# Performance work log

Measured on AMD Instinct MI355X. Metric: run time of the kernel, lower is better.

The kernel has to match this reference:

```python
import jax, jax.numpy as jnp
import numpy as np

B, N, C = 16, 1024, 256
NH, DH = 8, 32          # dense attention heads
NHD, P = 8, 4           # deformable heads / sampling points
Hs = Ws = 32            # value spatial grid (N == Hs*Ws)
HID = 1024              # mlp hidden = 4*C


def setup_inputs() -> dict:
    key = jax.random.key(0)
    ks = jax.random.split(key, 16)
    rn = lambda i, shape, s=1.0: jax.random.normal(ks[i], shape, jnp.float32) * s
    return {
        "x": rn(0, (B, N, C)),
        "ref": jax.random.uniform(ks[1], (B, N, 2), jnp.float32),
        "value": rn(2, (B, N, C)),
        "ln1_w": jnp.ones((C,), jnp.float32), "ln1_b": jnp.zeros((C,), jnp.float32),
        "ln2_w": jnp.ones((C,), jnp.float32), "ln2_b": jnp.zeros((C,), jnp.float32),
        "ln3_w": jnp.ones((C,), jnp.float32), "ln3_b": jnp.zeros((C,), jnp.float32),
        "qkv_w": rn(3, (3 * C, C), 0.05),
        "proj_w": rn(4, (C, C), 0.05), "proj_b": jnp.zeros((C,), jnp.float32),
        "off_w": rn(5, (NHD * P * 2, C), 0.01), "off_b": rn(6, (NHD * P * 2,), 0.5),
        "aw_w": rn(7, (NHD * P, C), 0.01), "aw_b": jnp.zeros((NHD * P,), jnp.float32),
        "vproj_w": rn(8, (C, C), 0.05), "vproj_b": jnp.zeros((C,), jnp.float32),
        "oproj_w": rn(9, (C, C), 0.05), "oproj_b": jnp.zeros((C,), jnp.float32),
        "fc1_w": rn(10, (HID, C), 0.05), "fc1_b": jnp.zeros((HID,), jnp.float32),
        "fc2_w": rn(11, (C, HID), 0.05), "fc2_b": jnp.zeros((C,), jnp.float32),
    }


def _ln(x, w, b):
    m = x.mean(-1, keepdims=True)
    v = ((x - m) ** 2).mean(-1, keepdims=True)
    return (x - m) * jax.lax.rsqrt(v + 1e-5) * w + b


def _attn(x, qkv_w, proj_w, proj_b):
    qkv = (x @ qkv_w.T).reshape(B, N, 3, NH, DH)
    q, k, v = qkv[:, :, 0], qkv[:, :, 1], qkv[:, :, 2]
    a = jnp.einsum('bqhd,bkhd->bhqk', q, k) * (DH ** -0.5)
    a = jax.nn.softmax(a, axis=-1)
    o = jnp.einsum('bhqk,bkhd->bqhd', a, v).reshape(B, N, C)
    return o @ proj_w.T + proj_b


def _deform(q, ref, value, off_w, off_b, aw_w, aw_b, vproj_w, vproj_b, oproj_w, oproj_b):
    # single-level MS deformable attention (Deformable-DETR style)
    v = (value @ vproj_w.T + vproj_b).reshape(B, Hs * Ws, NHD, DH)
    off = (q @ off_w.T + off_b).reshape(B, N, NHD, P, 2)
    aw = jax.nn.softmax((q @ aw_w.T + aw_b).reshape(B, N, NHD, P), axis=-1)
    norm = jnp.array([Ws, Hs], jnp.float32)
    loc = ref[:, :, None, None, :] + off / norm  # [B,N,NHD,P,2] normalized coords
    gx = loc[..., 0] * Ws - 0.5
    gy = loc[..., 1] * Hs - 0.5
    x0 = jnp.floor(gx); y0 = jnp.floor(gy)
    lx = gx - x0; ly = gy - y0
    x0i = x0.astype(jnp.int32); y0i = y0.astype(jnp.int32)
    b_idx = jnp.arange(B)[:, None, None, None]
    h_idx = jnp.arange(NHD)[None, None, :, None]

    def gather(xi, yi):
        valid = ((xi >= 0) & (xi < Ws) & (yi >= 0) & (yi < Hs)).astype(jnp.float32)
        idx = jnp.clip(yi, 0, Hs - 1) * Ws + jnp.clip(xi, 0, Ws - 1)
        return v[b_idx, idx, h_idx] * valid[..., None]  # [B,N,NHD,P,DH]

    s = (gather(x0i, y0i) * ((1 - lx) * (1 - ly))[..., None]
         + gather(x0i + 1, y0i) * (lx * (1 - ly))[..., None]
         + gather(x0i, y0i + 1) * ((1 - lx) * ly)[..., None]
         + gather(x0i + 1, y0i + 1) * (lx * ly)[..., None])
    out = (s * aw[..., None]).sum(axis=3).reshape(B, N, C)
    return out @ oproj_w.T + oproj_b


def reference(x, ref, value, ln1_w, ln1_b, ln2_w, ln2_b, ln3_w, ln3_b,
              qkv_w, proj_w, proj_b, off_w, off_b, aw_w, aw_b,
              vproj_w, vproj_b, oproj_w, oproj_b, fc1_w, fc1_b, fc2_w, fc2_b):
    x = x + _attn(_ln(x, ln1_w, ln1_b), qkv_w, proj_w, proj_b)
    x = x + _deform(_ln(x, ln2_w, ln2_b), ref, value,
                    off_w, off_b, aw_w, aw_b, vproj_w, vproj_b, oproj_w, oproj_b)
    h = jax.nn.gelu(_ln(x, ln3_w, ln3_b) @ fc1_w.T + fc1_b, approximate=False) @ fc2_w.T + fc2_b
    return x + h
```

## Files before the change

kernel.cpp:

```cpp
#include <hip/hip_runtime.h>
#include <hip/hip_bf16.h>

#define Bq   16
#define Nq   1024
#define Cq   256
#define NHq  8
#define DHq  32
#define HIDq 1024
#define BNq  (Bq * Nq)

typedef float f32x4 __attribute__((ext_vector_type(4)));
typedef short bf16x8 __attribute__((ext_vector_type(8)));
typedef unsigned short ushort_t;

__device__ __forceinline__ unsigned int f2bf(float f) {
    unsigned int u = __builtin_bit_cast(unsigned int, f);
    u = (u + 0x7fffu + ((u >> 16) & 1u)) >> 16;
    return u & 0xffffu;
}
__device__ __forceinline__ unsigned int packbf2(float a, float b) {
    unsigned int ua = __builtin_bit_cast(unsigned int, a) + 0x8000u;
    unsigned int ub = __builtin_bit_cast(unsigned int, b) + 0x8000u;
    return __builtin_amdgcn_perm(ub, ua, 0x07060302);
}
__device__ __forceinline__ unsigned int cvtpk_bf16(float lo, float hi) {
    unsigned int r;
    asm("v_cvt_pk_bf16_f32 %0, %1, %2" : "=v"(r) : "v"(lo), "v"(hi));
    return r;
}
__device__ __forceinline__ float gelu_t(float x) {
    float y = x * (0.7978845608028654f + 0.035677408136300125f * x * x);
    float e = __builtin_amdgcn_exp2f(y * 2.8853900817779268f);
    return x - x / (1.f + e);
}

typedef __attribute__((address_space(1))) const unsigned int* gas_u32;
typedef __attribute__((address_space(3))) unsigned int* las_u32;
__device__ __forceinline__ void gload16(const void* g, void* l) {
    __builtin_amdgcn_global_load_lds((gas_u32)g, (las_u32)l, 16, 0, 0);
}

struct CastSeg { const float* src; ushort_t* dst; int nblk; int n; };
struct CastArgs { CastSeg s[9]; };

__global__ __launch_bounds__(256) void castm(CastArgs a) {
    int bid = blockIdx.x;
    int seg = 0, acc = 0;
    for (seg = 0; seg < 9; seg++) {
        if (bid < acc + a.s[seg].nblk) break;
        acc += a.s[seg].nblk;
    }
    const CastSeg sg = a.s[seg];
    int i = (bid - acc) * 1024 + threadIdx.x * 4;
    if (i < sg.n) {
        float4 v = *(const float4*)(sg.src + i);
        uint2 u;
        u.x = packbf2(v.x, v.y);
        u.y = packbf2(v.z, v.w);
        *(uint2*)(sg.dst + i) = u;
    }
}

__global__ __launch_bounds__(256) void ln_kernel(const float* __restrict__ X,
                                                 const float* __restrict__ w,
                                                 const float* __restrict__ b,
                                                 ushort_t* __restrict__ Y) {
    int wave = threadIdx.x >> 6, lane = threadIdx.x & 63;
    int t = blockIdx.x * 4 + wave;
    float4 v = *(const float4*)(X + (size_t)t * Cq + lane * 4);
    float s = v.x + v.y + v.z + v.w;
#pragma unroll
    for (int d = 1; d < 64; d <<= 1) s += __shfl_xor(s, d);
    float mean = s * (1.f / 256.f);
    float4 dv = {v.x - mean, v.y - mean, v.z - mean, v.w - mean};
    float q = dv.x * dv.x + dv.y * dv.y + dv.z * dv.z + dv.w * dv.w;
#pragma unroll
    for (int d = 1; d < 64; d <<= 1) q += __shfl_xor(q, d);
    float rs = rsqrtf(q * (1.f / 256.f) + 1e-5f);
    float4 wv = *(const float4*)(w + lane * 4);
    float4 bv = *(const float4*)(b + lane * 4);
    uint2 u;
    u.x = packbf2(dv.x * rs * wv.x + bv.x, dv.y * rs * wv.y + bv.y);
    u.y = packbf2(dv.z * rs * wv.z + bv.z, dv.w * rs * wv.w + bv.w);
    *(uint2*)(Y + (size_t)t * Cq + lane * 4) = u;
}

template <int OMODE, bool GELU_, bool RESID, int KT>
__global__ __launch_bounds__(256) void mgemm(const ushort_t* __restrict__ A,
                                             const ushort_t* __restrict__ W,
                                             const float* __restrict__ bias,
                                             const float* __restrict__ R,
                                             void* __restrict__ OutP,
                                             int M, int Nn) {
    __shared__ __align__(16) ushort_t Al[2][8192];
    __shared__ __align__(16) ushort_t Bl[2][4096];
    int m0 = blockIdx.x * 128, n0 = blockIdx.y * 64;
    int tid = threadIdx.x;
    int w = tid >> 6, lane = tid & 63;
    int l15 = lane & 15, quad = lane >> 4;

    f32x4 acc[2][4];
#pragma unroll
    for (int i = 0; i < 2; i++)
#pragma unroll
        for (int j = 0; j < 4; j++) acc[i][j] = (f32x4){0.f, 0.f, 0.f, 0.f};

    const ushort_t* gA0 = A + (size_t)(m0 + lane) * KT + w * 8;
    const ushort_t* gA1 = gA0 + (size_t)64 * KT;
    const ushort_t* gB0 = W + (size_t)(n0 + lane) * KT + w * 8;

    auto STAGE = [&](int buf, int t) {
        const int k0 = t * 64;
        gload16(gA0 + k0,      &Al[buf][w * 1024]);
        gload16(gA1 + k0,      &Al[buf][w * 1024 + 512]);
        gload16(gA0 + k0 + 32, &Al[buf][(w + 4) * 1024]);
        gload16(gA1 + k0 + 32, &Al[buf][(w + 4) * 1024 + 512]);
        gload16(gB0 + k0,      &Bl[buf][w * 512]);
        gload16(gB0 + k0 + 32, &Bl[buf][(w + 4) * 512]);
    };

    constexpr int NT = KT / 64;
    STAGE(0, 0);
    STAGE(1, 1);
    asm volatile("s_waitcnt vmcnt(6)" ::: "memory");
    __builtin_amdgcn_s_barrier();

#pragma unroll
    for (int t = 0; t < NT; t++) {
        const int cur = t & 1;
        bf16x8 aF[2][2], bF[2][4];
#pragma unroll
        for (int ks = 0; ks < 2; ks++) {
#pragma unroll
            for (int i = 0; i < 2; i++)
                aF[ks][i] = *(const bf16x8*)&Al[cur][(ks * 4 + quad) * 1024 + (w * 32 + i * 16 + l15) * 8];
#pragma unroll
            for (int j = 0; j < 4; j++)
                bF[ks][j] = *(const bf16x8*)&Bl[cur][(ks * 4 + quad) * 512 + (j * 16 + l15) * 8];
        }
        asm volatile("s_waitcnt lgkmcnt(0)" ::: "memory");
        __builtin_amdgcn_sched_barrier(0);
        __builtin_amdgcn_s_barrier();
        if (t + 2 < NT) STAGE(cur, t + 2);

        __builtin_amdgcn_s_setprio(1);
#pragma unroll
        for (int ks = 0; ks < 2; ks++)
#pragma unroll
            for (int i = 0; i < 2; i++)
#pragma unroll
                for (int j = 0; j < 4; j++)
                    acc[i][j] = __builtin_amdgcn_mfma_f32_16x16x32_bf16(bF[ks][j], aF[ks][i], acc[i][j], 0, 0, 0);
        __builtin_amdgcn_s_setprio(0);

        if (t + 2 < NT) {
            asm volatile("s_waitcnt vmcnt(6)" ::: "memory");
        } else if (t + 1 < NT) {
            asm volatile("s_waitcnt vmcnt(0)" ::: "memory");
        }
        if (t + 1 < NT) __builtin_amdgcn_s_barrier();
    }

#pragma unroll
    for (int i = 0; i < 2; i++) {
        int mg = m0 + w * 32 + i * 16 + l15;
#pragma unroll
        for (int j = 0; j < 4; j++) {
            int ng = n0 + j * 16 + quad * 4;
            f32x4 rv = acc[i][j];
            if constexpr (OMODE == 1) {
                int which = ng >> 8;
                int h = (ng >> 5) & 7;
                int d = ng & 31;
                int bb = mg >> 10, nn = mg & 1023;
                ushort_t* qb = (ushort_t*)OutP;
                if (which == 2) {
                    size_t dst = 2 * (size_t)BNq * Cq +
                                 ((size_t)(bb * 8 + h) * 32 + d) * 1024 + nn;
#pragma unroll
                    for (int r = 0; r < 4; r++)
                        qb[dst + (size_t)r * 1024] = (ushort_t)f2bf(rv[r]);
                } else {
                    if (which == 0) {
                        const float sc = 0.17677669529663687f * 1.4426950408889634f;
                        rv[0] *= sc; rv[1] *= sc; rv[2] *= sc; rv[3] *= sc;
                    }
                    size_t dst = (size_t)which * ((size_t)BNq * Cq) +
                                 ((size_t)(bb * 8 + h) * 1024 + nn) * 32 + d;
                    uint2 pk;
                    pk.x = packbf2(rv[0], rv[1]);
                    pk.y = packbf2(rv[2], rv[3]);
                    *(uint2*)(qb + dst) = pk;
                }
            } else if constexpr (OMODE == 3) {
                if (ng >= 96) continue;
                if (ng < 64) {
                    float4 bv = *(const float4*)(bias + ng);
                    rv[0] += bv.x; rv[1] += bv.y; rv[2] += bv.z; rv[3] += bv.w;
                    *(float4*)((float*)OutP + (size_t)mg * 64 + ng) =
                        make_float4(rv[0], rv[1], rv[2], rv[3]);
                } else {
                    float4 bv = *(const float4*)(R + (ng - 64));
                    rv[0] += bv.x; rv[1] += bv.y; rv[2] += bv.z; rv[3] += bv.w;
                    *(float4*)((float*)OutP + (size_t)BNq * 64 + (size_t)mg * 32 + (ng - 64)) =
                        make_float4(rv[0], rv[1], rv[2], rv[3]);
                }
            } else {
                if (bias) {
                    float4 bv = *(const float4*)(bias + ng);
                    rv[0] += bv.x; rv[1] += bv.y; rv[2] += bv.z; rv[3] += bv.w;
                }
                if (GELU_) {
#pragma unroll
                    for (int r = 0; r < 4; r++) rv[r] = gelu_t(rv[r]);
                }
                if constexpr (OMODE == 2) {
                    uint2 pk;
                    pk.x = packbf2(rv[0], rv[1]);
                    pk.y = packbf2(rv[2], rv[3]);
                    *(uint2*)((ushort_t*)OutP + (size_t)mg * Nn + ng) = pk;
                } else {
                    if (RESID) {
                        float4 rr = *(const float4*)(R + (size_t)mg * Nn + ng);
                        rv[0] += rr.x; rv[1] += rr.y; rv[2] += rr.z; rv[3] += rr.w;
                    }
                    *(float4*)((float*)OutP + (size_t)mg * Nn + ng) =
                        make_float4(rv[0], rv[1], rv[2], rv[3]);
                }
            }
        }
    }
}

__global__ __launch_bounds__(256, 4) void attn_mfma(const ushort_t* __restrict__ Qb,
                                                    const ushort_t* __restrict__ Kb,
                                                    const ushort_t* __restrict__ Vtg,
                                                    ushort_t* __restrict__ o) {
    int bh = blockIdx.x;
    int b = bh >> 3, h = bh & 7;
    int q0 = blockIdx.y * 128;
    int tid = threadIdx.x;
    int wave = tid >> 6, lane = tid & 63;
    int l15 = lane & 15, quad = lane >> 4;

    __shared__ __align__(16) ushort_t Ks[2][64][40];
    __shared__ __align__(16) ushort_t Vs[2][32][88];
    __shared__ __align__(16) ushort_t Ps[4][32][72];

    const size_t hb = (size_t)bh * 32768;

    bf16x8 qfrag[2];
#pragma unroll
    for (int g = 0; g < 2; g++)
        qfrag[g] = *(const bf16x8*)(Qb + hb + (size_t)(q0 + wave * 32 + g * 16 + l15) * 32 + quad * 8);

    f32x4 oa[2][2];
#pragma unroll
    for (int g = 0; g < 2; g++)
#pragma unroll
        for (int t = 0; t < 2; t++) oa[g][t] = (f32x4){0.f, 0.f, 0.f, 0.f};
    f32x4 ls[2];
    ls[0] = (f32x4){0.f, 0.f, 0.f, 0.f};
    ls[1] = (f32x4){0.f, 0.f, 0.f, 0.f};

    bf16x8 ones;
#pragma unroll
    for (int i = 0; i < 8; i++) ones[i] = (short)0x3F80;

    int krow = tid >> 2, kch = tid & 3;
    int vrow = tid >> 3, vch = tid & 7;
    const ushort_t* kgp = Kb + hb + (size_t)krow * 32 + kch * 8;
    const ushort_t* vgp = Vtg + hb + (size_t)vrow * 1024 + vch * 8;

    bf16x8 kreg = *(const bf16x8*)kgp;
    bf16x8 vreg = *(const bf16x8*)vgp;

#pragma unroll 2
    for (int kt = 0; kt < 16; kt++) {
        const int cur = kt & 1;
        *(bf16x8*)&Ks[cur][krow][kch * 8] = kreg;
        *(bf16x8*)&Vs[cur][vrow][vch * 8] = vreg;
        __syncthreads();
        if (kt < 15) {
            kreg = *(const bf16x8*)(kgp + (kt + 1) * 2048);
            vreg = *(const bf16x8*)(vgp + (kt + 1) * 64);
        }

        bf16x8 kf[4];
#pragma unroll
        for (int kg = 0; kg < 4; kg++)
            kf[kg] = *(const bf16x8*)&Ks[cur][kg * 16 + l15][quad * 8];

        const f32x4 z = {0.f, 0.f, 0.f, 0.f};
#pragma unroll
        for (int g = 0; g < 2; g++) {
#pragma unroll
            for (int kg = 0; kg < 4; kg++) {
                f32x4 st = __builtin_amdgcn_mfma_f32_16x16x32_bf16(kf[kg], qfrag[g], z, 0, 0, 0);
                float e0 = __builtin_amdgcn_exp2f(st[0]);
                float e1 = __builtin_amdgcn_exp2f(st[1]);
                float e2 = __builtin_amdgcn_exp2f(st[2]);
                float e3 = __builtin_amdgcn_exp2f(st[3]);
                uint2 pk;
                pk.x = cvtpk_bf16(e0, e1);
                pk.y = cvtpk_bf16(e2, e3);
                *(uint2*)&Ps[wave][g * 16 + l15][kg * 16 + quad * 4] = pk;
            }
        }

        __builtin_amdgcn_s_setprio(1);
#pragma unroll
        for (int c = 0; c < 2; c++) {
            bf16x8 vb0 = *(const bf16x8*)&Vs[cur][l15][c * 32 + quad * 8];
            bf16x8 vb1 = *(const bf16x8*)&Vs[cur][16 + l15][c * 32 + quad * 8];
#pragma unroll
            for (int g = 0; g < 2; g++) {
                bf16x8 pa = *(const bf16x8*)&Ps[wave][g * 16 + l15][c * 32 + quad * 8];
                oa[g][0] = __builtin_amdgcn_mfma_f32_16x16x32_bf16(pa, vb0, oa[g][0], 0, 0, 0);
                oa[g][1] = __builtin_amdgcn_mfma_f32_16x16x32_bf16(pa, vb1, oa[g][1], 0, 0, 0);
                ls[g]    = __builtin_amdgcn_mfma_f32_16x16x32_bf16(pa, ones, ls[g], 0, 0, 0);
            }
        }
        __builtin_amdgcn_s_setprio(0);
    }

#pragma unroll
    for (int g = 0; g < 2; g++) {
#pragma unroll
        for (int r = 0; r < 4; r++) {
            float inv = 1.f / ls[g][r];
            int q = q0 + wave * 32 + g * 16 + quad * 4 + r;
            ushort_t* orow = o + ((size_t)(b * 1024 + q)) * 256 + h * 32;
            orow[l15] = (ushort_t)f2bf(oa[g][0][r] * inv);
            orow[l15 + 16] = (ushort_t)f2bf(oa[g][1][r] * inv);
        }
    }
}

__global__ __launch_bounds__(256) void deform_kernel(const float* __restrict__ ref,
                                                     const float* __restrict__ off,
                                                     const float* __restrict__ awl,
                                                     const float* __restrict__ v,
                                                     ushort_t* __restrict__ out) {
    int t = blockIdx.x;
    int b = t >> 10;
    int tid = threadIdx.x;
    int h = tid >> 5, d = tid & 31;

    float rx = ref[(size_t)t * 2 + 0];
    float ry = ref[(size_t)t * 2 + 1];
    const float* offr = off + (size_t)t * 64 + h * 8;
    const float* awr = awl + (size_t)t * 32 + h * 4;

    float L0 = awr[0], L1 = awr[1], L2 = awr[2], L3 = awr[3];
    float mm = fmaxf(fmaxf(L0, L1), fmaxf(L2, L3));
    float e0 = __expf(L0 - mm), e1 = __expf(L1 - mm), e2 = __expf(L2 - mm), e3 = __expf(L3 - mm);
    float inv = 1.f / (e0 + e1 + e2 + e3);
    float aw[4] = {e0 * inv, e1 * inv, e2 * inv, e3 * inv};

    const float* vb = v + (size_t)b * Nq * Cq + h * 32 + d;

    float s = 0.f;
#pragma unroll
    for (int p = 0; p < 4; p++) {
        float gx = rx * 32.f + offr[p * 2 + 0] - 0.5f;
        float gy = ry * 32.f + offr[p * 2 + 1] - 0.5f;
        float x0f = floorf(gx), y0f = floorf(gy);
        float lx = gx - x0f, ly = gy - y0f;
        int x0 = (int)x0f, y0 = (int)y0f;
        auto g = [&](int xi, int yi) -> float {
            if (xi < 0 || xi > 31 || yi < 0 || yi > 31) return 0.f;
            return vb[(size_t)(yi * 32 + xi) * Cq];
        };
        float sp = g(x0, y0) * (1.f - lx) * (1.f - ly)
                 + g(x0 + 1, y0) * lx * (1.f - ly)
                 + g(x0, y0 + 1) * (1.f - lx) * ly
                 + g(x0 + 1, y0 + 1) * lx * ly;
        s += aw[p] * sp;
    }
    out[(size_t)t * Cq + h * 32 + d] = (ushort_t)f2bf(s);
}

extern "C" void kernel_launch(void* const* d_in, const int* in_sizes, int n_in,
                              void* d_out, int out_size, void* d_ws, size_t ws_size,
                              hipStream_t stream) {
    const size_t S = (size_t)BNq * Cq;
    float* ws = (float*)d_ws;
    float* X = ws;
    ushort_t* Ybf = (ushort_t*)(ws + S);
    ushort_t* Wbf = (ushort_t*)(ws + S + S / 2);

    ushort_t* Wqkv   = Wbf;
    ushort_t* Wproj  = Wbf + 196608;
    ushort_t* Woff   = Wbf + 262144;
    ushort_t* Waw    = Wbf + 278528;
    ushort_t* Wvproj = Wbf + 286720;
    ushort_t* Woproj = Wbf + 352256;
    ushort_t* Wfc1   = Wbf + 417792;
    ushort_t* Wfc2   = Wbf + 679936;

    ushort_t* QKVbf = (ushort_t*)(ws + 2 * S);
    ushort_t* O1bf  = (ushort_t*)(ws + 2 * S + 3 * S / 2);
    float* Vb   = ws + 2 * S + S / 2;
    float* OffB = ws + 2 * S + 3 * S / 2;
    float* AwB  = OffB + (size_t)BNq * 64;
    ushort_t* Sbbf = (ushort_t*)(AwB + (size_t)BNq * 32);
    ushort_t* Hbbf = (ushort_t*)(ws + 2 * S);
    ushort_t* Valbf = (ushort_t*)(ws + 9 * S / 2);

    auto fp = [&](int i) { return (const float*)d_in[i]; };
    const float* x_in = fp(0);

    CastArgs ca;
    ca.s[0] = {fp(9),  Wqkv,   192, 196608};
    ca.s[1] = {fp(10), Wproj,  64,  65536};
    ca.s[2] = {fp(12), Woff,   16,  16384};
    ca.s[3] = {fp(14), Waw,    8,   8192};
    ca.s[4] = {fp(16), Wvproj, 64,  65536};
    ca.s[5] = {fp(18), Woproj, 64,  65536};
    ca.s[6] = {fp(20), Wfc1,   256, 262144};
    ca.s[7] = {fp(22), Wfc2,   256, 262144};
    ca.s[8] = {fp(2),  Valbf,  4096, (int)S};
    castm<<<5016, 256, 0, stream>>>(ca);

    ln_kernel<<<BNq / 4, 256, 0, stream>>>(x_in, fp(3), fp(4), Ybf);
    mgemm<1, false, false, 256><<<dim3(128, 12), 256, 0, stream>>>(
        Ybf, Wqkv, nullptr, nullptr, QKVbf, BNq, 768);
    attn_mfma<<<dim3(128, 8), 256, 0, stream>>>(
        QKVbf, QKVbf + S, QKVbf + 2 * S, O1bf);
    mgemm<0, false, true, 256><<<dim3(128, 4), 256, 0, stream>>>(
        O1bf, Wproj, fp(11), x_in, X, BNq, 256);

    ln_kernel<<<BNq / 4, 256, 0, stream>>>(X, fp(5), fp(6), Ybf);
    mgemm<0, false, false, 256><<<dim3(128, 4), 256, 0, stream>>>(
        Valbf, Wvproj, fp(17), nullptr, Vb, BNq, 256);
    mgemm<3, false, false, 256><<<dim3(128, 2), 256, 0, stream>>>(
        Ybf, Woff, fp(13), fp(15), OffB, BNq, 96);
    deform_kernel<<<BNq, 256, 0, stream>>>(fp(1), OffB, AwB, Vb, Sbbf);
    mgemm<0, false, true, 256><<<dim3(128, 4), 256, 0, stream>>>(
        Sbbf, Woproj, fp(19), X, X, BNq, 256);

    ln_kernel<<<BNq / 4, 256, 0, stream>>>(X, fp(7), fp(8), Ybf);
    mgemm<2, true, false, 256><<<dim3(128, 16), 256, 0, stream>>>(
        Ybf, Wfc1, fp(21), nullptr, Hbbf, BNq, 1024);
    mgemm<0, false, true, 1024><<<dim3(128, 4), 256, 0, stream>>>(
        Hbbf, Wfc2, fp(23), X, d_out, BNq, 256);
}
```

Baseline: 332.2 us.

## Replace double-buffered GEMM k-loop with large single-stage 256-wide K chunks

The GEMM mainloop drops the two-stage LDS double buffer with explicit vmcnt waits. It now loads an entire 256-wide K chunk of A and W into LDS, synchronises, then runs eight MFMA substeps from LDS. This cuts barriers and wait bookkeeping per K, but global loads no longer overlap compute within a block. LDS use grows to 96 KB, which may reduce occupancy.

```diff
diff --git a/kernel.cpp b/kernel.cpp
--- a/kernel.cpp
+++ b/kernel.cpp
@@ -92,8 +92,8 @@
                                              const float* __restrict__ R,
                                              void* __restrict__ OutP,
                                              int M, int Nn) {
-    __shared__ __align__(16) ushort_t Al[2][8192];
-    __shared__ __align__(16) ushort_t Bl[2][4096];
+    __shared__ __align__(16) ushort_t Al[32768];
+    __shared__ __align__(16) ushort_t Bl[16384];
     int m0 = blockIdx.x * 128, n0 = blockIdx.y * 64;
     int tid = threadIdx.x;
     int w = tid >> 6, lane = tid & 63;
@@ -105,60 +105,43 @@
 #pragma unroll
         for (int j = 0; j < 4; j++) acc[i][j] = (f32x4){0.f, 0.f, 0.f, 0.f};
 
-    const ushort_t* gA0 = A + (size_t)(m0 + lane) * KT + w * 8;
+    const ushort_t* gA0 = A + (size_t)(m0 + lane) * KT;
     const ushort_t* gA1 = gA0 + (size_t)64 * KT;
-    const ushort_t* gB0 = W + (size_t)(n0 + lane) * KT + w * 8;
-
-    auto STAGE = [&](int buf, int t) {
-        const int k0 = t * 64;
-        gload16(gA0 + k0,      &Al[buf][w * 1024]);
-        gload16(gA1 + k0,      &Al[buf][w * 1024 + 512]);
-        gload16(gA0 + k0 + 32, &Al[buf][(w + 4) * 1024]);
-        gload16(gA1 + k0 + 32, &Al[buf][(w + 4) * 1024 + 512]);
-        gload16(gB0 + k0,      &Bl[buf][w * 512]);
-        gload16(gB0 + k0 + 32, &Bl[buf][(w + 4) * 512]);
-    };
-
-    constexpr int NT = KT / 64;
-    STAGE(0, 0);
-    STAGE(1, 1);
-    asm volatile("s_waitcnt vmcnt(6)" ::: "memory");
-    __builtin_amdgcn_s_barrier();
-
-#pragma unroll
-    for (int t = 0; t < NT; t++) {
-        const int cur = t & 1;
-        bf16x8 aF[2][2], bF[2][4];
-#pragma unroll
-        for (int ks = 0; ks < 2; ks++) {
+    const ushort_t* gB0 = W + (size_t)(n0 + lane) * KT;
+
+    constexpr int NC = KT / 256;
+#pragma unroll
+    for (int c = 0; c < NC; c++) {
+        if (c > 0) __syncthreads();
+        const int kb = c * 256;
+#pragma unroll
+        for (int j = 0; j < 8; j++) {
+            const int k = kb + w * 8 + j * 32;
+            const int kc = w + 4 * j;
+            gload16(gA0 + k, &Al[kc * 1024]);
+            gload16(gA1 + k, &Al[kc * 1024 + 512]);
+            gload16(gB0 + k, &Bl[kc * 512]);
+        }
+        __syncthreads();
+
+        __builtin_amdgcn_s_setprio(1);
+#pragma unroll
+        for (int s = 0; s < 8; s++) {
+            const int kc = 4 * s + quad;
+            bf16x8 aF[2], bF[4];
 #pragma unroll
             for (int i = 0; i < 2; i++)
-                aF[ks][i] = *(const bf16x8*)&Al[cur][(ks * 4 + quad) * 1024 + (w * 32 + i * 16 + l15) * 8];
+                aF[i] = *(const bf16x8*)&Al[kc * 1024 + (w * 32 + i * 16 + l15) * 8];
 #pragma unroll
             for (int j = 0; j < 4; j++)
-                bF[ks][j] = *(const bf16x8*)&Bl[cur][(ks * 4 + quad) * 512 + (j * 16 + l15) * 8];
-        }
-        asm volatile("s_waitcnt lgkmcnt(0)" ::: "memory");
-        __builtin_amdgcn_sched_barrier(0);
-        __builtin_amdgcn_s_barrier();
-        if (t + 2 < NT) STAGE(cur, t + 2);
-
-        __builtin_amdgcn_s_setprio(1);
-#pragma unroll
-        for (int ks = 0; ks < 2; ks++)
+                bF[j] = *(const bf16x8*)&Bl[kc * 512 + (j * 16 + l15) * 8];
 #pragma unroll
             for (int i = 0; i < 2; i++)
 #pragma unroll
                 for (int j = 0; j < 4; j++)
-                    acc[i][j] = __builtin_amdgcn_mfma_f32_16x16x32_bf16(bF[ks][j], aF[ks][i], acc[i][j], 0, 0, 0);
+                    acc[i][j] = __builtin_amdgcn_mfma_f32_16x16x32_bf16(bF[j], aF[i], acc[i][j], 0, 0, 0);
+        }
         __builtin_amdgcn_s_setprio(0);
-
-        if (t + 2 < NT) {
-            asm volatile("s_waitcnt vmcnt(6)" ::: "memory");
-        } else if (t + 1 < NT) {
-            asm volatile("s_waitcnt vmcnt(0)" ::: "memory");
-        }
-        if (t + 1 < NT) __builtin_amdgcn_s_barrier();
     }
 
 #pragma unroll
```

After: 377.3 us. 1.14x slower.

## Triple-buffer GEMM LDS pipeline and remap block IDs per XCD

Applied to the files above, without the earlier changes.

The shared mgemm kernel moves from double to triple-buffered LDS staging, prefetching three K-tiles ahead and adjusting vmcnt waits to match. It also switches to a 1D grid with an XCD-aware remap, so the 16 consecutive M-tiles handled by each XCD share weight tiles in that XCD's L2. The aim is to hide more global load latency and improve cache locality. The cost is 50% more LDS per block, which may lower occupancy. With KT=256 there are only four K-tiles, so the deeper prefetch gives little room to overlap.

```diff
diff --git a/kernel.cpp b/kernel.cpp
--- a/kernel.cpp
+++ b/kernel.cpp
@@ -12,6 +12,10 @@
 typedef float f32x4 __attribute__((ext_vector_type(4)));
 typedef short bf16x8 __attribute__((ext_vector_type(8)));
 typedef unsigned short ushort_t;
+
+#define VMW12() asm volatile("s_waitcnt vmcnt(12)" ::: "memory")
+#define VMW6()  asm volatile("s_waitcnt vmcnt(6)" ::: "memory")
+#define VMW0()  asm volatile("s_waitcnt vmcnt(0)" ::: "memory")
 
 __device__ __forceinline__ unsigned int f2bf(float f) {
     unsigned int u = __builtin_bit_cast(unsigned int, f);
@@ -92,9 +96,13 @@
                                              const float* __restrict__ R,
                                              void* __restrict__ OutP,
                                              int M, int Nn) {
-    __shared__ __align__(16) ushort_t Al[2][8192];
-    __shared__ __align__(16) ushort_t Bl[2][4096];
-    int m0 = blockIdx.x * 128, n0 = blockIdx.y * 64;
+    __shared__ __align__(16) ushort_t Al[3][8192];
+    __shared__ __align__(16) ushort_t Bl[3][4096];
+    int L = blockIdx.x;
+    int xcd = L & 7, idx = L >> 3;
+    int bx = xcd * 16 + (idx & 15);
+    int by = idx >> 4;
+    int m0 = bx * 128, n0 = by * 64;
     int tid = threadIdx.x;
     int w = tid >> 6, lane = tid & 63;
     int l15 = lane & 15, quad = lane >> 4;
@@ -122,12 +130,14 @@
     constexpr int NT = KT / 64;
     STAGE(0, 0);
     STAGE(1, 1);
-    asm volatile("s_waitcnt vmcnt(6)" ::: "memory");
+    STAGE(2, 2);
+    VMW12();
     __builtin_amdgcn_s_barrier();
+    __builtin_amdgcn_sched_barrier(0);
 
 #pragma unroll
     for (int t = 0; t < NT; t++) {
-        const int cur = t & 1;
+        const int cur = t % 3;
         bf16x8 aF[2][2], bF[2][4];
 #pragma unroll
         for (int ks = 0; ks < 2; ks++) {
@@ -141,7 +151,8 @@
         asm volatile("s_waitcnt lgkmcnt(0)" ::: "memory");
         __builtin_amdgcn_sched_barrier(0);
         __builtin_amdgcn_s_barrier();
-        if (t + 2 < NT) STAGE(cur, t + 2);
+        __builtin_amdgcn_sched_barrier(0);
+        if (t + 3 < NT) STAGE(cur, t + 3);
 
         __builtin_amdgcn_s_setprio(1);
 #pragma unroll
@@ -153,12 +164,14 @@
                     acc[i][j] = __builtin_amdgcn_mfma_f32_16x16x32_bf16(bF[ks][j], aF[ks][i], acc[i][j], 0, 0, 0);
         __builtin_amdgcn_s_setprio(0);
 
-        if (t + 2 < NT) {
-            asm volatile("s_waitcnt vmcnt(6)" ::: "memory");
-        } else if (t + 1 < NT) {
-            asm volatile("s_waitcnt vmcnt(0)" ::: "memory");
-        }
-        if (t + 1 < NT) __builtin_amdgcn_s_barrier();
+        if (t + 1 < NT) {
+            const int rem = ((t + 3 < NT ? t + 3 : NT - 1)) - (t + 1);
+            if (rem >= 2)      { VMW12(); }
+            else if (rem == 1) { VMW6(); }
+            else               { VMW0(); }
+            __builtin_amdgcn_s_barrier();
+            __builtin_amdgcn_sched_barrier(0);
+        }
     }
 
 #pragma unroll
@@ -424,25 +437,25 @@
     castm<<<5016, 256, 0, stream>>>(ca);
 
     ln_kernel<<<BNq / 4, 256, 0, stream>>>(x_in, fp(3), fp(4), Ybf);
-    mgemm<1, false, false, 256><<<dim3(128, 12), 256, 0, stream>>>(
+    mgemm<1, false, false, 256><<<128 * 12, 256, 0, stream>>>(
         Ybf, Wqkv, nullptr, nullptr, QKVbf, BNq, 768);
     attn_mfma<<<dim3(128, 8), 256, 0, stream>>>(
         QKVbf, QKVbf + S, QKVbf + 2 * S, O1bf);
-    mgemm<0, false, true, 256><<<dim3(128, 4), 256, 0, stream>>>(
+    mgemm<0, false, true, 256><<<128 * 4, 256, 0, stream>>>(
         O1bf, Wproj, fp(11), x_in, X, BNq, 256);
 
     ln_kernel<<<BNq / 4, 256, 0, stream>>>(X, fp(5), fp(6), Ybf);
-    mgemm<0, false, false, 256><<<dim3(128, 4), 256, 0, stream>>>(
+    mgemm<0, false, false, 256><<<128 * 4, 256, 0, stream>>>(
         Valbf, Wvproj, fp(17), nullptr, Vb, BNq, 256);
-    mgemm<3, false, false, 256><<<dim3(128, 2), 256, 0, stream>>>(
+    mgemm<3, false, false, 256><<<128 * 2, 256, 0, stream>>>(
         Ybf, Woff, fp(13), fp(15), OffB, BNq, 96);
     deform_kernel<<<BNq, 256, 0, stream>>>(fp(1), OffB, AwB, Vb, Sbbf);
-    mgemm<0, false, true, 256><<<dim3(128, 4), 256, 0, stream>>>(
+    mgemm<0, false, true, 256><<<128 * 4, 256, 0, stream>>>(
         Sbbf, Woproj, fp(19), X, X, BNq, 256);
 
     ln_kernel<<<BNq / 4, 256, 0, stream>>>(X, fp(7), fp(8), Ybf);
-    mgemm<2, true, false, 256><<<dim3(128, 16), 256, 0, stream>>>(
+    mgemm<2, true, false, 256><<<128 * 16, 256, 0, stream>>>(
         Ybf, Wfc1, fp(21), nullptr, Hbbf, BNq, 1024);
-    mgemm<0, false, true, 1024><<<dim3(128, 4), 256, 0, stream>>>(
+    mgemm<0, false, true, 1024><<<128 * 4, 256, 0, stream>>>(
         Hbbf, Wfc2, fp(23), X, d_out, BNq, 256);
 }
```

New measurement: 339.3 us. 2.1% more time.

## Process multiple M-tiles per GEMM block with continuous cross-tile prefetch pipeline

Applied to the files above, without the earlier changes.

The mgemm kernel gains an NTILES template parameter so each block processes several consecutive 128-row M tiles. The double-buffered load pipeline runs across tile boundaries, so loads for the next tile are issued while the current one finishes and its epilogue runs. The QKV GEMM uses 2 tiles per block and fc1 uses 4, which shrinks their grids. This is meant to amortise pipeline prologue/drain and launch overhead, at the cost of fewer blocks and therefore less parallelism across the GPU.

```diff
diff --git a/kernel.cpp b/kernel.cpp
--- a/kernel.cpp
+++ b/kernel.cpp
@@ -12,6 +12,9 @@
 typedef float f32x4 __attribute__((ext_vector_type(4)));
 typedef short bf16x8 __attribute__((ext_vector_type(8)));
 typedef unsigned short ushort_t;
+
+#define VMW6()  asm volatile("s_waitcnt vmcnt(6)" ::: "memory")
+#define VMW0()  asm volatile("s_waitcnt vmcnt(0)" ::: "memory")
 
 __device__ __forceinline__ unsigned int f2bf(float f) {
     unsigned int u = __builtin_bit_cast(unsigned int, f);
@@ -85,7 +88,7 @@
     *(uint2*)(Y + (size_t)t * Cq + lane * 4) = u;
 }
 
-template <int OMODE, bool GELU_, bool RESID, int KT>
+template <int OMODE, bool GELU_, bool RESID, int KT, int NTILES>
 __global__ __launch_bounds__(256) void mgemm(const ushort_t* __restrict__ A,
                                              const ushort_t* __restrict__ W,
                                              const float* __restrict__ bias,
@@ -94,7 +97,9 @@
                                              int M, int Nn) {
     __shared__ __align__(16) ushort_t Al[2][8192];
     __shared__ __align__(16) ushort_t Bl[2][4096];
-    int m0 = blockIdx.x * 128, n0 = blockIdx.y * 64;
+    constexpr int NT = KT / 64;
+    constexpr int TOT = NT * NTILES;
+    int m_base = blockIdx.x * (128 * NTILES), n0 = blockIdx.y * 64;
     int tid = threadIdx.x;
     int w = tid >> 6, lane = tid & 63;
     int l15 = lane & 15, quad = lane >> 4;
@@ -105,29 +110,101 @@
 #pragma unroll
         for (int j = 0; j < 4; j++) acc[i][j] = (f32x4){0.f, 0.f, 0.f, 0.f};
 
-    const ushort_t* gA0 = A + (size_t)(m0 + lane) * KT + w * 8;
+    const ushort_t* gA0 = A + (size_t)(m_base + lane) * KT + w * 8;
     const ushort_t* gA1 = gA0 + (size_t)64 * KT;
     const ushort_t* gB0 = W + (size_t)(n0 + lane) * KT + w * 8;
 
-    auto STAGE = [&](int buf, int t) {
-        const int k0 = t * 64;
-        gload16(gA0 + k0,      &Al[buf][w * 1024]);
-        gload16(gA1 + k0,      &Al[buf][w * 1024 + 512]);
-        gload16(gA0 + k0 + 32, &Al[buf][(w + 4) * 1024]);
-        gload16(gA1 + k0 + 32, &Al[buf][(w + 4) * 1024 + 512]);
-        gload16(gB0 + k0,      &Bl[buf][w * 512]);
-        gload16(gB0 + k0 + 32, &Bl[buf][(w + 4) * 512]);
+    auto STAGE = [&](int buf, int u) {
+        const size_t aoff = (size_t)(u / NT) * 128 * KT + (u % NT) * 64;
+        const int k0 = (u % NT) * 64;
+        gload16(gA0 + aoff,      &Al[buf][w * 1024]);
+        gload16(gA1 + aoff,      &Al[buf][w * 1024 + 512]);
+        gload16(gA0 + aoff + 32, &Al[buf][(w + 4) * 1024]);
+        gload16(gA1 + aoff + 32, &Al[buf][(w + 4) * 1024 + 512]);
+        gload16(gB0 + k0,        &Bl[buf][w * 512]);
+        gload16(gB0 + k0 + 32,   &Bl[buf][(w + 4) * 512]);
     };
 
-    constexpr int NT = KT / 64;
+    auto EPI = [&](int tile) {
+#pragma unroll
+        for (int i = 0; i < 2; i++) {
+            int mg = m_base + tile * 128 + w * 32 + i * 16 + l15;
+#pragma unroll
+            for (int j = 0; j < 4; j++) {
+                int ng = n0 + j * 16 + quad * 4;
+                f32x4 rv = acc[i][j];
+                if constexpr (OMODE == 1) {
+                    int which = ng >> 8;
+                    int h = (ng >> 5) & 7;
+                    int d = ng & 31;
+                    int bb = mg >> 10, nn = mg & 1023;
+                    ushort_t* qb = (ushort_t*)OutP;
+                    if (which == 2) {
+                        size_t dst = 2 * (size_t)BNq * Cq +
+                                     ((size_t)(bb * 8 + h) * 32 + d) * 1024 + nn;
+#pragma unroll
+                        for (int r = 0; r < 4; r++)
+                            qb[dst + (size_t)r * 1024] = (ushort_t)f2bf(rv[r]);
+                    } else {
+                        if (which == 0) {
+                            const float sc = 0.17677669529663687f * 1.4426950408889634f;
+                            rv[0] *= sc; rv[1] *= sc; rv[2] *= sc; rv[3] *= sc;
+                        }
+                        size_t dst = (size_t)which * ((size_t)BNq * Cq) +
+                                     ((size_t)(bb * 8 + h) * 1024 + nn) * 32 + d;
+                        uint2 pk;
+                        pk.x = packbf2(rv[0], rv[1]);
+                        pk.y = packbf2(rv[2], rv[3]);
+                        *(uint2*)(qb + dst) = pk;
+                    }
+                } else if constexpr (OMODE == 3) {
+                    if (ng >= 96) continue;
+                    if (ng < 64) {
+                        float4 bv = *(const float4*)(bias + ng);
+                        rv[0] += bv.x; rv[1] += bv.y; rv[2] += bv.z; rv[3] += bv.w;
+                        *(float4*)((float*)OutP + (size_t)mg * 64 + ng) =
+                            make_float4(rv[0], rv[1], rv[2], rv[3]);
+                    } else {
+                        float4 bv = *(const float4*)(R + (ng - 64));
+                        rv[0] += bv.x; rv[1] += bv.y; rv[2] += bv.z; rv[3] += bv.w;
+                        *(float4*)((float*)OutP + (size_t)BNq * 64 + (size_t)mg * 32 + (ng - 64)) =
+                            make_float4(rv[0], rv[1], rv[2], rv[3]);
+                    }
+                } else {
+                    if (bias) {
+                        float4 bv = *(const float4*)(bias + ng);
+                        rv[0] += bv.x; rv[1] += bv.y; rv[2] += bv.z; rv[3] += bv.w;
+                    }
+                    if (GELU_) {
+#pragma unroll
+                        for (int r = 0; r < 4; r++) rv[r] = gelu_t(rv[r]);
+                    }
+                    if constexpr (OMODE == 2) {
+                        uint2 pk;
+                        pk.x = packbf2(rv[0], rv[1]);
+                        pk.y = packbf2(rv[2], rv[3]);
+                        *(uint2*)((ushort_t*)OutP + (size_t)mg * Nn + ng) = pk;
+                    } else {
+                        if (RESID) {
+                            float4 rr = *(const float4*)(R + (size_t)mg * Nn + ng);
+                            rv[0] += rr.x; rv[1] += rr.y; rv[2] += rr.z; rv[3] += rr.w;
+                        }
+                        *(float4*)((float*)OutP + (size_t)mg * Nn + ng) =
+                            make_float4(rv[0], rv[1], rv[2], rv[3]);
+                    }
+                }
+            }
+        }
+    };
+
     STAGE(0, 0);
     STAGE(1, 1);
-    asm volatile("s_waitcnt vmcnt(6)" ::: "memory");
+    VMW6();
     __builtin_amdgcn_s_barrier();
 
 #pragma unroll
-    for (int t = 0; t < NT; t++) {
-        const int cur = t & 1;
+    for (int s = 0; s < TOT; s++) {
+        const int cur = s & 1;
         bf16x8 aF[2][2], bF[2][4];
 #pragma unroll
         for (int ks = 0; ks < 2; ks++) {
@@ -141,7 +218,7 @@
         asm volatile("s_waitcnt lgkmcnt(0)" ::: "memory");
         __builtin_amdgcn_sched_barrier(0);
         __builtin_amdgcn_s_barrier();
-        if (t + 2 < NT) STAGE(cur, t + 2);
+        if (s + 2 < TOT) STAGE(cur, s + 2);
 
         __builtin_amdgcn_s_setprio(1);
 #pragma unroll
@@ -153,81 +230,15 @@
                     acc[i][j] = __builtin_amdgcn_mfma_f32_16x16x32_bf16(bF[ks][j], aF[ks][i], acc[i][j], 0, 0, 0);
         __builtin_amdgcn_s_setprio(0);
 
-        if (t + 2 < NT) {
-            asm volatile("s_waitcnt vmcnt(6)" ::: "memory");
-        } else if (t + 1 < NT) {
-            asm volatile("s_waitcnt vmcnt(0)" ::: "memory");
-        }
-        if (t + 1 < NT) __builtin_amdgcn_s_barrier();
-    }
-
-#pragma unroll
-    for (int i = 0; i < 2; i++) {
-        int mg = m0 + w * 32 + i * 16 + l15;
-#pragma unroll
-        for (int j = 0; j < 4; j++) {
-            int ng = n0 + j * 16 + quad * 4;
-            f32x4 rv = acc[i][j];
-            if constexpr (OMODE == 1) {
-                int which = ng >> 8;
-                int h = (ng >> 5) & 7;
-                int d = ng & 31;
-                int bb = mg >> 10, nn = mg & 1023;
-                ushort_t* qb = (ushort_t*)OutP;
-                if (which == 2) {
-                    size_t dst = 2 * (size_t)BNq * Cq +
-                                 ((size_t)(bb * 8 + h) * 32 + d) * 1024 + nn;
-#pragma unroll
-                    for (int r = 0; r < 4; r++)
-                        qb[dst + (size_t)r * 1024] = (ushort_t)f2bf(rv[r]);
-                } else {
-                    if (which == 0) {
-                        const float sc = 0.17677669529663687f * 1.4426950408889634f;
-                        rv[0] *= sc; rv[1] *= sc; rv[2] *= sc; rv[3] *= sc;
-                    }
-                    size_t dst = (size_t)which * ((size_t)BNq * Cq) +
-                                 ((size_t)(bb * 8 + h) * 1024 + nn) * 32 + d;
-                    uint2 pk;
-                    pk.x = packbf2(rv[0], rv[1]);
-                    pk.y = packbf2(rv[2], rv[3]);
-                    *(uint2*)(qb + dst) = pk;
-                }
-            } else if constexpr (OMODE == 3) {
-                if (ng >= 96) continue;
-                if (ng < 64) {
-                    float4 bv = *(const float4*)(bias + ng);
-                    rv[0] += bv.x; rv[1] += bv.y; rv[2] += bv.z; rv[3] += bv.w;
-                    *(float4*)((float*)OutP + (size_t)mg * 64 + ng) =
-                        make_float4(rv[0], rv[1], rv[2], rv[3]);
-                } else {
-                    float4 bv = *(const float4*)(R + (ng - 64));
-                    rv[0] += bv.x; rv[1] += bv.y; rv[2] += bv.z; rv[3] += bv.w;
-                    *(float4*)((float*)OutP + (size_t)BNq * 64 + (size_t)mg * 32 + (ng - 64)) =
-                        make_float4(rv[0], rv[1], rv[2], rv[3]);
-                }
-            } else {
-                if (bias) {
-                    float4 bv = *(const float4*)(bias + ng);
-                    rv[0] += bv.x; rv[1] += bv.y; rv[2] += bv.z; rv[3] += bv.w;
-                }
-                if (GELU_) {
-#pragma unroll
-                    for (int r = 0; r < 4; r++) rv[r] = gelu_t(rv[r]);
-                }
-                if constexpr (OMODE == 2) {
-                    uint2 pk;
-                    pk.x = packbf2(rv[0], rv[1]);
-                    pk.y = packbf2(rv[2], rv[3]);
-                    *(uint2*)((ushort_t*)OutP + (size_t)mg * Nn + ng) = pk;
-                } else {
-                    if (RESID) {
-                        float4 rr = *(const float4*)(R + (size_t)mg * Nn + ng);
-                        rv[0] += rr.x; rv[1] += rr.y; rv[2] += rr.z; rv[3] += rr.w;
-                    }
-                    *(float4*)((float*)OutP + (size_t)mg * Nn + ng) =
-                        make_float4(rv[0], rv[1], rv[2], rv[3]);
-                }
-            }
+        if (s + 2 < TOT)      { VMW6(); __builtin_amdgcn_s_barrier(); }
+        else if (s + 1 < TOT) { VMW0(); __builtin_amdgcn_s_barrier(); }
+
+        if ((s + 1) % NT == 0) {
+            EPI((s + 1) / NT - 1);
+#pragma unroll
+            for (int i = 0; i < 2; i++)
+#pragma unroll
+                for (int j = 0; j < 4; j++) acc[i][j] = (f32x4){0.f, 0.f, 0.f, 0.f};
         }
     }
 }
@@ -424,25 +435,25 @@
     castm<<<5016, 256, 0, stream>>>(ca);
 
     ln_kernel<<<BNq / 4, 256, 0, stream>>>(x_in, fp(3), fp(4), Ybf);
-    mgemm<1, false, false, 256><<<dim3(128, 12), 256, 0, stream>>>(
+    mgemm<1, false, false, 256, 2><<<dim3(64, 12), 256, 0, stream>>>(
         Ybf, Wqkv, nullptr, nullptr, QKVbf, BNq, 768);
     attn_mfma<<<dim3(128, 8), 256, 0, stream>>>(
         QKVbf, QKVbf + S, QKVbf + 2 * S, O1bf);
-    mgemm<0, false, true, 256><<<dim3(128, 4), 256, 0, stream>>>(
+    mgemm<0, false, true, 256, 1><<<dim3(128, 4), 256, 0, stream>>>(
         O1bf, Wproj, fp(11), x_in, X, BNq, 256);
 
     ln_kernel<<<BNq / 4, 256, 0, stream>>>(X, fp(5), fp(6), Ybf);
-    mgemm<0, false, false, 256><<<dim3(128, 4), 256, 0, stream>>>(
+    mgemm<0, false, false, 256, 1><<<dim3(128, 4), 256, 0, stream>>>(
         Valbf, Wvproj, fp(17), nullptr, Vb, BNq, 256);
-    mgemm<3, false, false, 256><<<dim3(128, 2), 256, 0, stream>>>(
+    mgemm<3, false, false, 256, 1><<<dim3(128, 2), 256, 0, stream>>>(
         Ybf, Woff, fp(13), fp(15), OffB, BNq, 96);
     deform_kernel<<<BNq, 256, 0, stream>>>(fp(1), OffB, AwB, Vb, Sbbf);
-    mgemm<0, false, true, 256><<<dim3(128, 4), 256, 0, stream>>>(
+    mgemm<0, false, true, 256, 1><<<dim3(128, 4), 256, 0, stream>>>(
         Sbbf, Woproj, fp(19), X, X, BNq, 256);
 
     ln_kernel<<<BNq / 4, 256, 0, stream>>>(X, fp(7), fp(8), Ybf);
-    mgemm<2, true, false, 256><<<dim3(128, 16), 256, 0, stream>>>(
+    mgemm<2, true, false, 256, 4><<<dim3(32, 16), 256, 0, stream>>>(
         Ybf, Wfc1, fp(21), nullptr, Hbbf, BNq, 1024);
-    mgemm<0, false, true, 1024><<<dim3(128, 4), 256, 0, stream>>>(
+    mgemm<0, false, true, 1024, 1><<<dim3(128, 4), 256, 0, stream>>>(
         Hbbf, Wfc2, fp(23), X, d_out, BNq, 256);
 }
```

Result: slower. 341.1 us (+2.7%).
